# Optimization experiments

Measured on AMD Instinct MI355X. Metric: run time of the kernel, lower is better.

The kernel has to match this reference:

```python
import jax, jax.numpy as jnp
import numpy as np

B, H, L = 1024, 32, 3
D_S, D_ID = 512, 128
D_STEER = 3 * D_S + D_ID  # 1664
D_HID = 2048
HS, DQ = 16, 64
HDQ = HS * DQ  # 1024


def setup_inputs() -> dict:
    key = jax.random.key(0)
    ks = jax.random.split(key, 18)
    n = lambda k, shape, std: jax.random.normal(k, shape, dtype=jnp.float32) * std
    inp = {
        "x": jax.random.normal(ks[0], (B * H, D_STEER), dtype=jnp.float32),
        "id_in": jax.random.normal(ks[1], (B * H, D_ID), dtype=jnp.float32),
        # per-head content MLP params
        "in_proj_w": n(ks[2], (H, D_STEER, D_S), 0.014),
        "in_proj_b": jnp.zeros((H, D_S), jnp.float32),
        "norm_w": jnp.ones((H, L, D_S), jnp.float32),
        "up_w": n(ks[3], (H, L, D_S, D_HID), 0.014),
        "up_b": jnp.zeros((H, L, D_HID), jnp.float32),
        "down_w": n(ks[4], (H, L, D_HID, D_S), (2.0 / D_HID) ** 0.5),
        "down_b": jnp.zeros((H, L, D_S), jnp.float32),
        # q_proj: Linear(D_steer, 2*HDQ) -> GELU -> Linear(2*HDQ, HDQ)
        "q1_w": n(ks[5], (D_STEER, 2 * HDQ), 0.014),
        "q1_b": jnp.zeros((2 * HDQ,), jnp.float32),
        "q2_w": n(ks[6], (2 * HDQ, HDQ), 0.02),
        "q2_b": jnp.zeros((HDQ,), jnp.float32),
        # k_proj: Linear(D_id, 2*HDQ) -> GELU -> Linear(2*HDQ, HDQ)
        "k1_w": n(ks[7], (D_ID, 2 * HDQ), 0.014),
        "k1_b": jnp.zeros((2 * HDQ,), jnp.float32),
        "k2_w": n(ks[8], (2 * HDQ, HDQ), 0.02),
        "k2_b": jnp.zeros((HDQ,), jnp.float32),
    }
    return inp


def _per_head_mlp(x, in_proj_w, in_proj_b, norm_w, up_w, up_b, down_w, down_b):
    # x: [B*H, D_steer] -> [B*H, D_s]
    bh = x.shape[0]
    b = bh // H
    xh = x.reshape(b, H, D_STEER)
    h = jnp.einsum("bhd,hde->bhe", xh, in_proj_w) + in_proj_b[None]
    for i in range(norm_w.shape[1]):
        rms = jax.lax.rsqrt(jnp.mean(h * h, axis=-1, keepdims=True) + 1e-6)
        xn = h * rms * norm_w[:, i][None]
        hid = jax.nn.gelu(jnp.einsum("bhd,hde->bhe", xn, up_w[:, i]) + up_b[:, i][None], approximate=False)
        h = h + jnp.einsum("bhd,hde->bhe", hid, down_w[:, i]) + down_b[:, i][None]
    return h.reshape(bh, D_S)


def reference(x, id_in, in_proj_w, in_proj_b, norm_w, up_w, up_b, down_w, down_b,
              q1_w, q1_b, q2_w, q2_b, k1_w, k1_b, k2_w, k2_b):
    content = _per_head_mlp(x, in_proj_w, in_proj_b, norm_w, up_w, up_b, down_w, down_b)
    q = jax.nn.gelu(x @ q1_w + q1_b, approximate=False) @ q2_w + q2_b
    k = jax.nn.gelu(id_in @ k1_w + k1_b, approximate=False) @ k2_w + k2_b
    # concat outputs: [B*H, D_s + HDQ + HDQ]
    return jnp.concatenate([content, q, k], axis=-1)
```

## Files before the change

### kernel.cpp

```cpp
#include <hip/hip_runtime.h>
#include <hip/hip_bf16.h>
#include <math.h>

#define HH 32
#define LL 3
#define DS 512
#define DID 128
#define DSTEER 1664
#define DHID 2048
#define HDQ 1024
#define BHROWS 32768

typedef __attribute__((ext_vector_type(8))) short short8;
typedef __attribute__((ext_vector_type(4))) float f32x4;

typedef const __attribute__((address_space(1))) unsigned int* gptr_t;
typedef __attribute__((address_space(3))) unsigned int* lptr_t;

#define FENCE() asm volatile("" ::: "memory")
#define BAR() do { FENCE(); __builtin_amdgcn_s_barrier(); FENCE(); } while (0)
#define VMCNT10() asm volatile("s_waitcnt vmcnt(10)" ::: "memory")
#define VMCNT8()  asm volatile("s_waitcnt vmcnt(8)" ::: "memory")
#define VMCNT2()  asm volatile("s_waitcnt vmcnt(2)" ::: "memory")
#define VMCNT0()  asm volatile("s_waitcnt vmcnt(0)" ::: "memory")

__device__ __forceinline__ unsigned short f2bf(float f) {
  union { float f; unsigned int u; } x; x.f = f;
  unsigned int r = (x.u + 0x7FFFu + ((x.u >> 16) & 1u)) >> 16;
  return (unsigned short)r;
}
__device__ __forceinline__ unsigned int pk2(float a, float b) {
  return (unsigned int)f2bf(a) | ((unsigned int)f2bf(b) << 16);
}
__device__ __forceinline__ float gelu_exact(float v) {
  return 0.5f * v * (1.0f + erff(v * 0.70710678118654752440f));
}

__global__ void cvt_bf16_kernel(const float4* __restrict__ in, uint2* __restrict__ out, long n4) {
  long i = (long)blockIdx.x * blockDim.x + threadIdx.x;
  long stride = (long)gridDim.x * blockDim.x;
  for (; i < n4; i += stride) {
    float4 v = in[i];
    uint2 o; o.x = pk2(v.x, v.y); o.y = pk2(v.z, v.w);
    out[i] = o;
  }
}

__global__ void transpose_cvt_kernel(const float* __restrict__ in, long long in_bstride,
                                     unsigned short* __restrict__ out, long long out_bstride,
                                     int R, int C) {
  __shared__ float t[64][33];
  const int r0 = blockIdx.y * 32;
  const int c0 = blockIdx.x * 64;
  const float* bin = in + (long long)blockIdx.z * in_bstride;
  unsigned short* bout = out + (long long)blockIdx.z * out_bstride;
  const int tid = threadIdx.x;
  const int col = tid & 63, rr = tid >> 6;
  #pragma unroll
  for (int j = 0; j < 8; j++) {
    int r = j * 4 + rr;
    t[col][r] = bin[(size_t)(r0 + r) * C + c0 + col];
  }
  __syncthreads();
  const int rq = (tid & 7) * 4;
  const int cc = tid >> 3;
  #pragma unroll
  for (int j = 0; j < 2; j++) {
    int c = j * 32 + cc;
    float v0 = t[c][rq], v1 = t[c][rq + 1], v2 = t[c][rq + 2], v3 = t[c][rq + 3];
    uint2 o; o.x = pk2(v0, v1); o.y = pk2(v2, v3);
    *(uint2*)&bout[(size_t)(c0 + c) * R + r0 + rq] = o;
  }
}

__global__ void rms_scale_kernel(const float* __restrict__ h,
                                 const float* __restrict__ norm_w,
                                 unsigned short* __restrict__ xn, int layer) {
  int gw = (int)((blockIdx.x * blockDim.x + threadIdx.x) >> 6);
  int lane = threadIdx.x & 63;
  if (gw >= BHROWS) return;
  int head = gw & (HH - 1);
  const float4* hr = (const float4*)(h + (size_t)gw * DS);
  float4 v0 = hr[lane * 2], v1 = hr[lane * 2 + 1];
  float ss = v0.x*v0.x + v0.y*v0.y + v0.z*v0.z + v0.w*v0.w
           + v1.x*v1.x + v1.y*v1.y + v1.z*v1.z + v1.w*v1.w;
  #pragma unroll
  for (int off = 32; off > 0; off >>= 1) ss += __shfl_xor(ss, off, 64);
  float r = rsqrtf(ss * (1.0f / DS) + 1e-6f);
  const float4* nw = (const float4*)(norm_w + ((size_t)head * LL + layer) * DS);
  float4 w0 = nw[lane * 2], w1 = nw[lane * 2 + 1];
  uint4 o;
  o.x = pk2(v0.x * r * w0.x, v0.y * r * w0.y);
  o.y = pk2(v0.z * r * w0.z, v0.w * r * w0.w);
  o.z = pk2(v1.x * r * w1.x, v1.y * r * w1.y);
  o.w = pk2(v1.z * r * w1.z, v1.w * r * w1.w);
  *(uint4*)(xn + (size_t)gw * DS + (size_t)lane * 8) = o;
}

template<int EPI>
__global__ __launch_bounds__(512, 2)
void gemm256_kernel(const unsigned short* __restrict__ A, int lda, int rstep,
                    const unsigned short* __restrict__ Bt, int ldb, long long b_hstride,
                    const float* __restrict__ bias, int bias_hstride,
                    const float* __restrict__ resid, int ldr,
                    void* __restrict__ Cv, int ldc, int K) {
  __shared__ unsigned short lds[2 * 2 * 256 * 64];
  const int tid = threadIdx.x;
  const int lane = tid & 63;
  const int wave = tid >> 6;
  const int wr = wave >> 2, wc = wave & 3;
  const int head = blockIdx.z;
  const int gx = gridDim.x;
  const int nwg = gx * gridDim.y;
  int wgid = blockIdx.y * gx + blockIdx.x;
  { int cpx = nwg >> 3; wgid = (wgid & 7) * cpx + (wgid >> 3); }
  const int tn = wgid % gx, tm = wgid / gx;

  const int l3 = lane >> 3;
  const int gslot = ((lane & 7) ^ l3) * 8;
  const int mbase = wave * 8 + l3;
  const int nbase = (wave >> 2) * 64 + (wave & 3) * 8 + l3;
  const unsigned short* pA = A + ((size_t)(tm * 256 + mbase) * rstep + head) * lda + gslot;
  const unsigned short* pB = Bt + (size_t)head * b_hstride
                               + (size_t)(tn * 256 + nbase) * ldb + gslot;
  const size_t aBlk = (size_t)64 * rstep * lda;

  const int physk0 = ((lane >> 4) ^ (lane & 7)) * 8;
  const int physk1 = ((4 + (lane >> 4)) ^ (lane & 7)) * 8;
  const int aRow = wr * 128 + (lane & 15);
  const int bRow = wc * 32 + (lane & 15);

  auto stageA = [&](unsigned short* dstA, int h, size_t kels) {
    #pragma unroll
    for (int i = 0; i < 2; ++i)
      __builtin_amdgcn_global_load_lds(
          (gptr_t)(pA + (size_t)(i * 2 + h) * aBlk + kels),
          (lptr_t)(dstA + ((i * 2 + h) * 64 + wave * 8) * 64), 16, 0, 0);
  };
  auto stageB = [&](unsigned short* dstB, int h, size_t kels) {
    #pragma unroll
    for (int i = 0; i < 2; ++i)
      __builtin_amdgcn_global_load_lds(
          (gptr_t)(pB + (size_t)(i * 128 + h * 32) * ldb + kels),
          (lptr_t)(dstB + (h * 128 + i * 64 + wave * 8) * 64), 16, 0, 0);
  };

  f32x4 acc[8][4];
  #pragma unroll
  for (int i = 0; i < 8; ++i)
    #pragma unroll
    for (int j = 0; j < 4; ++j) acc[i][j] = (f32x4){0.f, 0.f, 0.f, 0.f};
  short8 a[4][2], b[4][2];

  const int T = K >> 6;
  stageA(lds, 0, 0);
  stageB(lds + 16384, 0, 0);
  stageB(lds + 16384, 1, 0);
  stageA(lds, 1, 0);
  if (1 < T) {
    stageA(lds + 32768, 0, 64);
    stageB(lds + 32768 + 16384, 0, 64);
    stageB(lds + 32768 + 16384, 1, 64);
    VMCNT8();
  } else {
    VMCNT2();
  }
  BAR();

  for (int t = 0; t < T; ++t) {
    unsigned short* rA = lds + (t & 1) * 32768;
    unsigned short* rB = rA + 16384;
    unsigned short* nA = lds + ((t + 1) & 1) * 32768;
    unsigned short* cA = rA;
    unsigned short* cB = rB;
    const size_t k1 = (size_t)(t + 1) * 64;
    const size_t k2 = (size_t)(t + 2) * 64;
    const bool m1 = (t + 1 < T), m2 = (t + 2 < T);

    #pragma unroll
    for (int i = 0; i < 4; ++i) {
      a[i][0] = *(const short8*)&rA[(aRow + i * 16) * 64 + physk0];
      a[i][1] = *(const short8*)&rA[(aRow + i * 16) * 64 + physk1];
    }
    #pragma unroll
    for (int j = 0; j < 2; ++j) {
      b[j][0] = *(const short8*)&rB[(bRow + j * 16) * 64 + physk0];
      b[j][1] = *(const short8*)&rB[(bRow + j * 16) * 64 + physk1];
    }
    if (m1) stageA(nA, 1, k1);
    BAR();
    __builtin_amdgcn_s_setprio(1);
    #pragma unroll
    for (int i = 0; i < 4; ++i)
      #pragma unroll
      for (int j = 0; j < 2; ++j) {
        acc[i][j] = __builtin_amdgcn_mfma_f32_16x16x32_bf16(a[i][0], b[j][0], acc[i][j], 0, 0, 0);
        acc[i][j] = __builtin_amdgcn_mfma_f32_16x16x32_bf16(a[i][1], b[j][1], acc[i][j], 0, 0, 0);
      }
    __builtin_amdgcn_s_setprio(0);
    BAR();

    #pragma unroll
    for (int j = 0; j < 2; ++j) {
      b[2 + j][0] = *(const short8*)&rB[(128 + bRow + j * 16) * 64 + physk0];
      b[2 + j][1] = *(const short8*)&rB[(128 + bRow + j * 16) * 64 + physk1];
    }
    if (m2) stageA(cA, 0, k2);
    BAR();
    __builtin_amdgcn_s_setprio(1);
    #pragma unroll
    for (int i = 0; i < 4; ++i)
      #pragma unroll
      for (int j = 0; j < 2; ++j) {
        acc[i][2 + j] = __builtin_amdgcn_mfma_f32_16x16x32_bf16(a[i][0], b[2 + j][0], acc[i][2 + j], 0, 0, 0);
        acc[i][2 + j] = __builtin_amdgcn_mfma_f32_16x16x32_bf16(a[i][1], b[2 + j][1], acc[i][2 + j], 0, 0, 0);
      }
    __builtin_amdgcn_s_setprio(0);
    if (m2) { VMCNT10(); } else if (m1) { VMCNT8(); } else { VMCNT0(); }
    BAR();

    #pragma unroll
    for (int i = 0; i < 4; ++i) {
      a[i][0] = *(const short8*)&rA[(aRow + (4 + i) * 16) * 64 + physk0];
      a[i][1] = *(const short8*)&rA[(aRow + (4 + i) * 16) * 64 + physk1];
    }
    if (m2) stageB(cB, 0, k2);
    BAR();
    __builtin_amdgcn_s_setprio(1);
    #pragma unroll
    for (int i = 0; i < 4; ++i)
      #pragma unroll
      for (int j = 0; j < 2; ++j) {
        acc[4 + i][2 + j] = __builtin_amdgcn_mfma_f32_16x16x32_bf16(a[i][0], b[2 + j][0], acc[4 + i][2 + j], 0, 0, 0);
        acc[4 + i][2 + j] = __builtin_amdgcn_mfma_f32_16x16x32_bf16(a[i][1], b[2 + j][1], acc[4 + i][2 + j], 0, 0, 0);
      }
    __builtin_amdgcn_s_setprio(0);
    BAR();

    if (m2) stageB(cB, 1, k2);
    BAR();
    __builtin_amdgcn_s_setprio(1);
    #pragma unroll
    for (int i = 0; i < 4; ++i)
      #pragma unroll
      for (int j = 0; j < 2; ++j) {
        acc[4 + i][j] = __builtin_amdgcn_mfma_f32_16x16x32_bf16(a[i][0], b[j][0], acc[4 + i][j], 0, 0, 0);
        acc[4 + i][j] = __builtin_amdgcn_mfma_f32_16x16x32_bf16(a[i][1], b[j][1], acc[4 + i][j], 0, 0, 0);
      }
    __builtin_amdgcn_s_setprio(0);
    if (m1) { if (m2) { VMCNT8(); } else { VMCNT2(); } }
    BAR();
  }

  const float* bptr = bias + (size_t)head * bias_hstride;
  #pragma unroll
  for (int i = 0; i < 8; ++i) {
    #pragma unroll
    for (int j = 0; j < 4; ++j) {
      #pragma unroll
      for (int r = 0; r < 4; ++r) {
        int rowt = wr * 128 + i * 16 + (lane >> 4) * 4 + r;
        int colt = wc * 64 + j * 16 + (lane & 15);
        int col = tn * 256 + colt;
        size_t crow = (size_t)(tm * 256 + rowt) * rstep + head;
        float v = acc[i][j][r] + bptr[col];
        if (EPI == 1) {
          ((unsigned short*)Cv)[crow * (size_t)ldc + col] = f2bf(gelu_exact(v));
        } else if (EPI == 2) {
          v += resid[crow * (size_t)ldr + col];
          ((float*)Cv)[crow * (size_t)ldc + col] = v;
        } else {
          ((float*)Cv)[crow * (size_t)ldc + col] = v;
        }
      }
    }
  }
}

extern "C" void kernel_launch(void* const* d_in, const int* in_sizes, int n_in,
                              void* d_out, int out_size, void* d_ws, size_t ws_size,
                              hipStream_t stream) {
  const float* x         = (const float*)d_in[0];
  const float* id_in     = (const float*)d_in[1];
  const float* in_proj_w = (const float*)d_in[2];
  const float* in_proj_b = (const float*)d_in[3];
  const float* norm_w    = (const float*)d_in[4];
  const float* up_w      = (const float*)d_in[5];
  const float* up_b      = (const float*)d_in[6];
  const float* down_w    = (const float*)d_in[7];
  const float* down_b    = (const float*)d_in[8];
  const float* q1_w      = (const float*)d_in[9];
  const float* q1_b      = (const float*)d_in[10];
  const float* q2_w      = (const float*)d_in[11];
  const float* q2_b      = (const float*)d_in[12];
  const float* k1_w      = (const float*)d_in[13];
  const float* k1_b      = (const float*)d_in[14];
  const float* k2_w      = (const float*)d_in[15];
  const float* k2_b      = (const float*)d_in[16];
  float* out = (float*)d_out;

  char* ws = (char*)d_ws;
  unsigned short* x_bf  = (unsigned short*)ws; ws += (size_t)BHROWS * DSTEER * 2;
  unsigned short* id_bf = (unsigned short*)ws; ws += (size_t)BHROWS * DID * 2;
  float*          hbuf  = (float*)ws;          ws += (size_t)BHROWS * DS * 4;
  unsigned short* xn    = (unsigned short*)ws; ws += (size_t)BHROWS * DS * 2;
  unsigned short* hid   = (unsigned short*)ws; ws += (size_t)BHROWS * DHID * 2;
  unsigned short* wbuf  = (unsigned short*)ws; ws += (size_t)HH * DHID * DS * 2;

  cvt_bf16_kernel<<<2048, 256, 0, stream>>>((const float4*)x, (uint2*)x_bf,
                                            (long)BHROWS * DSTEER / 4);
  cvt_bf16_kernel<<<512, 256, 0, stream>>>((const float4*)id_in, (uint2*)id_bf,
                                           (long)BHROWS * DID / 4);

  transpose_cvt_kernel<<<dim3(2 * HDQ / 64, DSTEER / 32, 1), 256, 0, stream>>>(
      q1_w, 0, wbuf, 0, DSTEER, 2 * HDQ);
  gemm256_kernel<1><<<dim3(8, 128, 1), 512, 0, stream>>>(
      x_bf, DSTEER, 1, wbuf, DSTEER, 0, q1_b, 0, nullptr, 0, hid, 2 * HDQ, DSTEER);
  transpose_cvt_kernel<<<dim3(HDQ / 64, 2 * HDQ / 32, 1), 256, 0, stream>>>(
      q2_w, 0, wbuf, 0, 2 * HDQ, HDQ);
  gemm256_kernel<0><<<dim3(4, 128, 1), 512, 0, stream>>>(
      hid, 2 * HDQ, 1, wbuf, 2 * HDQ, 0, q2_b, 0, nullptr, 0, out + 512, 2560, 2 * HDQ);

  transpose_cvt_kernel<<<dim3(2 * HDQ / 64, DID / 32, 1), 256, 0, stream>>>(
      k1_w, 0, wbuf, 0, DID, 2 * HDQ);
  gemm256_kernel<1><<<dim3(8, 128, 1), 512, 0, stream>>>(
      id_bf, DID, 1, wbuf, DID, 0, k1_b, 0, nullptr, 0, hid, 2 * HDQ, DID);
  transpose_cvt_kernel<<<dim3(HDQ / 64, 2 * HDQ / 32, 1), 256, 0, stream>>>(
      k2_w, 0, wbuf, 0, 2 * HDQ, HDQ);
  gemm256_kernel<0><<<dim3(4, 128, 1), 512, 0, stream>>>(
      hid, 2 * HDQ, 1, wbuf, 2 * HDQ, 0, k2_b, 0, nullptr, 0, out + 1536, 2560, 2 * HDQ);

  transpose_cvt_kernel<<<dim3(DS / 64, DSTEER / 32, HH), 256, 0, stream>>>(
      in_proj_w, (long long)DSTEER * DS, wbuf, (long long)DS * DSTEER, DSTEER, DS);
  gemm256_kernel<0><<<dim3(2, 4, 32), 512, 0, stream>>>(
      x_bf, DSTEER, HH, wbuf, DSTEER, (long long)DS * DSTEER, in_proj_b, DS,
      nullptr, 0, hbuf, DS, DSTEER);

  for (int i = 0; i < LL; i++) {
    rms_scale_kernel<<<8192, 256, 0, stream>>>(hbuf, norm_w, xn, i);
    transpose_cvt_kernel<<<dim3(DHID / 64, DS / 32, HH), 256, 0, stream>>>(
        up_w + (size_t)i * DS * DHID, (long long)LL * DS * DHID,
        wbuf, (long long)DHID * DS, DS, DHID);
    gemm256_kernel<1><<<dim3(8, 4, 32), 512, 0, stream>>>(
        xn, DS, HH, wbuf, DS, (long long)DHID * DS,
        up_b + (size_t)i * DHID, LL * DHID, nullptr, 0, hid, DHID, DS);
    transpose_cvt_kernel<<<dim3(DS / 64, DHID / 32, HH), 256, 0, stream>>>(
        down_w + (size_t)i * DHID * DS, (long long)LL * DHID * DS,
        wbuf, (long long)DS * DHID, DHID, DS);
    float* cout = (i < 2) ? hbuf : out;
    int ldc = (i < 2) ? DS : 2560;
    gemm256_kernel<2><<<dim3(2, 4, 32), 512, 0, stream>>>(
        hid, DHID, HH, wbuf, DHID, (long long)DS * DHID,
        down_b + (size_t)i * DS, LL * DS, hbuf, DS, cout, ldc, DHID);
  }
}
```

Measured before the change: 1.726 ms.

## Software-pipeline LDS fragment loads across MFMA quadrants with register double-buffering

Restructures the GEMM main loop so LDS fragment reads for the next quadrant or next K-tile are issued before the current quadrant's MFMAs. Fine-grained lgkmcnt waits and sched barriers let ds_read latency hide behind matrix math. The loop is unrolled by two with ping-pong B-fragment registers, and the prologue and epilogue tiles are peeled with hand-tuned vmcnt thresholds. This adds register pressure. It also assumes an even tile count of at least two, and the vmcnt accounting must exactly match the outstanding global-to-LDS loads.

```diff
diff --git a/kernel.cpp b/kernel.cpp
--- a/kernel.cpp
+++ b/kernel.cpp
@@ -19,10 +19,13 @@
 
 #define FENCE() asm volatile("" ::: "memory")
 #define BAR() do { FENCE(); __builtin_amdgcn_s_barrier(); FENCE(); } while (0)
-#define VMCNT10() asm volatile("s_waitcnt vmcnt(10)" ::: "memory")
 #define VMCNT8()  asm volatile("s_waitcnt vmcnt(8)" ::: "memory")
+#define VMCNT4()  asm volatile("s_waitcnt vmcnt(4)" ::: "memory")
 #define VMCNT2()  asm volatile("s_waitcnt vmcnt(2)" ::: "memory")
 #define VMCNT0()  asm volatile("s_waitcnt vmcnt(0)" ::: "memory")
+#define VMNOP()   do {} while (0)
+#define LGKM(n) do { asm volatile("s_waitcnt lgkmcnt(" #n ")" ::: "memory"); \
+                     __builtin_amdgcn_sched_barrier(0); } while (0)
 
 __device__ __forceinline__ unsigned short f2bf(float f) {
   union { float f; unsigned int u; } x; x.f = f;
@@ -150,107 +153,102 @@
   for (int i = 0; i < 8; ++i)
     #pragma unroll
     for (int j = 0; j < 4; ++j) acc[i][j] = (f32x4){0.f, 0.f, 0.f, 0.f};
-  short8 a[4][2], b[4][2];
+  short8 aA[4][2], aB[4][2], bA[2][2], bB[2][2];
+
+#define MFMA_Q(MO, NO, AR, BR) do { \
+    __builtin_amdgcn_s_setprio(1); \
+    _Pragma("unroll") \
+    for (int i_ = 0; i_ < 4; ++i_) { \
+      _Pragma("unroll") \
+      for (int j_ = 0; j_ < 2; ++j_) { \
+        acc[(MO)+i_][(NO)+j_] = __builtin_amdgcn_mfma_f32_16x16x32_bf16( \
+            AR[i_][0], BR[j_][0], acc[(MO)+i_][(NO)+j_], 0, 0, 0); \
+        acc[(MO)+i_][(NO)+j_] = __builtin_amdgcn_mfma_f32_16x16x32_bf16( \
+            AR[i_][1], BR[j_][1], acc[(MO)+i_][(NO)+j_], 0, 0, 0); \
+      } \
+    } \
+    __builtin_amdgcn_s_setprio(0); \
+  } while (0)
+
+#define TILE(tt, LO, HI, PAR, M1, M2, VMP0, VMP2, VMP3) { \
+    unsigned short* rA = lds + (PAR) * 32768; \
+    unsigned short* rB = rA + 16384; \
+    unsigned short* nA = lds + ((PAR) ^ 1) * 32768; \
+    unsigned short* nB = nA + 16384; \
+    const size_t k1_ = (size_t)((tt) + 1) * 64; \
+    const size_t k2_ = (size_t)((tt) + 2) * 64; \
+     \
+    HI[0][0] = *(const short8*)&rB[(128 + bRow) * 64 + physk0]; \
+    HI[0][1] = *(const short8*)&rB[(128 + bRow) * 64 + physk1]; \
+    HI[1][0] = *(const short8*)&rB[(144 + bRow) * 64 + physk0]; \
+    HI[1][1] = *(const short8*)&rB[(144 + bRow) * 64 + physk1]; \
+    if (M1) stageA(nA, 1, k1_); \
+    LGKM(4); \
+    MFMA_Q(0, 0, aA, LO); \
+    VMP0; BAR(); \
+     \
+    _Pragma("unroll") \
+    for (int i_ = 0; i_ < 4; ++i_) { \
+      aB[i_][0] = *(const short8*)&rA[(aRow + (4 + i_) * 16) * 64 + physk0]; \
+      aB[i_][1] = *(const short8*)&rA[(aRow + (4 + i_) * 16) * 64 + physk1]; \
+    } \
+    if (M2) stageA(rA, 0, k2_); \
+    LGKM(8); \
+    MFMA_Q(0, 2, aA, HI); \
+    BAR(); \
+     \
+    if (M2) stageB(rB, 0, k2_); \
+    LGKM(0); \
+    MFMA_Q(4, 2, aB, HI); \
+    VMP2; BAR(); \
+     \
+    if (M1) { \
+      _Pragma("unroll") \
+      for (int i_ = 0; i_ < 4; ++i_) { \
+        aA[i_][0] = *(const short8*)&nA[(aRow + i_ * 16) * 64 + physk0]; \
+        aA[i_][1] = *(const short8*)&nA[(aRow + i_ * 16) * 64 + physk1]; \
+      } \
+      HI[0][0] = *(const short8*)&nB[(bRow) * 64 + physk0]; \
+      HI[0][1] = *(const short8*)&nB[(bRow) * 64 + physk1]; \
+      HI[1][0] = *(const short8*)&nB[(bRow + 16) * 64 + physk0]; \
+      HI[1][1] = *(const short8*)&nB[(bRow + 16) * 64 + physk1]; \
+      __builtin_amdgcn_sched_barrier(0); \
+    } \
+    if (M2) stageB(rB, 1, k2_); \
+    MFMA_Q(4, 0, aB, LO); \
+    VMP3; BAR(); \
+  }
 
   const int T = K >> 6;
   stageA(lds, 0, 0);
   stageB(lds + 16384, 0, 0);
   stageB(lds + 16384, 1, 0);
+  VMCNT0();
+  BAR();
+  #pragma unroll
+  for (int i = 0; i < 4; ++i) {
+    aA[i][0] = *(const short8*)&lds[(aRow + i * 16) * 64 + physk0];
+    aA[i][1] = *(const short8*)&lds[(aRow + i * 16) * 64 + physk1];
+  }
+  bA[0][0] = *(const short8*)&lds[(16384 / 1) + 0];
+  bA[0][0] = *(const short8*)&lds[16384 + (bRow) * 64 + physk0];
+  bA[0][1] = *(const short8*)&lds[16384 + (bRow) * 64 + physk1];
+  bA[1][0] = *(const short8*)&lds[16384 + (bRow + 16) * 64 + physk0];
+  bA[1][1] = *(const short8*)&lds[16384 + (bRow + 16) * 64 + physk1];
   stageA(lds, 1, 0);
-  if (1 < T) {
-    stageA(lds + 32768, 0, 64);
-    stageB(lds + 32768 + 16384, 0, 64);
-    stageB(lds + 32768 + 16384, 1, 64);
-    VMCNT8();
-  } else {
-    VMCNT2();
-  }
-  BAR();
-
-  for (int t = 0; t < T; ++t) {
-    unsigned short* rA = lds + (t & 1) * 32768;
-    unsigned short* rB = rA + 16384;
-    unsigned short* nA = lds + ((t + 1) & 1) * 32768;
-    unsigned short* cA = rA;
-    unsigned short* cB = rB;
-    const size_t k1 = (size_t)(t + 1) * 64;
-    const size_t k2 = (size_t)(t + 2) * 64;
-    const bool m1 = (t + 1 < T), m2 = (t + 2 < T);
-
-    #pragma unroll
-    for (int i = 0; i < 4; ++i) {
-      a[i][0] = *(const short8*)&rA[(aRow + i * 16) * 64 + physk0];
-      a[i][1] = *(const short8*)&rA[(aRow + i * 16) * 64 + physk1];
-    }
-    #pragma unroll
-    for (int j = 0; j < 2; ++j) {
-      b[j][0] = *(const short8*)&rB[(bRow + j * 16) * 64 + physk0];
-      b[j][1] = *(const short8*)&rB[(bRow + j * 16) * 64 + physk1];
-    }
-    if (m1) stageA(nA, 1, k1);
-    BAR();
-    __builtin_amdgcn_s_setprio(1);
-    #pragma unroll
-    for (int i = 0; i < 4; ++i)
-      #pragma unroll
-      for (int j = 0; j < 2; ++j) {
-        acc[i][j] = __builtin_amdgcn_mfma_f32_16x16x32_bf16(a[i][0], b[j][0], acc[i][j], 0, 0, 0);
-        acc[i][j] = __builtin_amdgcn_mfma_f32_16x16x32_bf16(a[i][1], b[j][1], acc[i][j], 0, 0, 0);
-      }
-    __builtin_amdgcn_s_setprio(0);
-    BAR();
-
-    #pragma unroll
-    for (int j = 0; j < 2; ++j) {
-      b[2 + j][0] = *(const short8*)&rB[(128 + bRow + j * 16) * 64 + physk0];
-      b[2 + j][1] = *(const short8*)&rB[(128 + bRow + j * 16) * 64 + physk1];
-    }
-    if (m2) stageA(cA, 0, k2);
-    BAR();
-    __builtin_amdgcn_s_setprio(1);
-    #pragma unroll
-    for (int i = 0; i < 4; ++i)
-      #pragma unroll
-      for (int j = 0; j < 2; ++j) {
-        acc[i][2 + j] = __builtin_amdgcn_mfma_f32_16x16x32_bf16(a[i][0], b[2 + j][0], acc[i][2 + j], 0, 0, 0);
-        acc[i][2 + j] = __builtin_amdgcn_mfma_f32_16x16x32_bf16(a[i][1], b[2 + j][1], acc[i][2 + j], 0, 0, 0);
-      }
-    __builtin_amdgcn_s_setprio(0);
-    if (m2) { VMCNT10(); } else if (m1) { VMCNT8(); } else { VMCNT0(); }
-    BAR();
-
-    #pragma unroll
-    for (int i = 0; i < 4; ++i) {
-      a[i][0] = *(const short8*)&rA[(aRow + (4 + i) * 16) * 64 + physk0];
-      a[i][1] = *(const short8*)&rA[(aRow + (4 + i) * 16) * 64 + physk1];
-    }
-    if (m2) stageB(cB, 0, k2);
-    BAR();
-    __builtin_amdgcn_s_setprio(1);
-    #pragma unroll
-    for (int i = 0; i < 4; ++i)
-      #pragma unroll
-      for (int j = 0; j < 2; ++j) {
-        acc[4 + i][2 + j] = __builtin_amdgcn_mfma_f32_16x16x32_bf16(a[i][0], b[2 + j][0], acc[4 + i][2 + j], 0, 0, 0);
-        acc[4 + i][2 + j] = __builtin_amdgcn_mfma_f32_16x16x32_bf16(a[i][1], b[2 + j][1], acc[4 + i][2 + j], 0, 0, 0);
-      }
-    __builtin_amdgcn_s_setprio(0);
-    BAR();
-
-    if (m2) stageB(cB, 1, k2);
-    BAR();
-    __builtin_amdgcn_s_setprio(1);
-    #pragma unroll
-    for (int i = 0; i < 4; ++i)
-      #pragma unroll
-      for (int j = 0; j < 2; ++j) {
-        acc[4 + i][j] = __builtin_amdgcn_mfma_f32_16x16x32_bf16(a[i][0], b[j][0], acc[4 + i][j], 0, 0, 0);
-        acc[4 + i][j] = __builtin_amdgcn_mfma_f32_16x16x32_bf16(a[i][1], b[j][1], acc[4 + i][j], 0, 0, 0);
-      }
-    __builtin_amdgcn_s_setprio(0);
-    if (m1) { if (m2) { VMCNT8(); } else { VMCNT2(); } }
-    BAR();
-  }
+  stageA(lds + 32768, 0, 64);
+  stageB(lds + 32768 + 16384, 0, 64);
+  stageB(lds + 32768 + 16384, 1, 64);
+
+  for (int t = 0; t + 3 < T; t += 2) {
+    TILE(t,     bA, bB, 0, 1, 1, VMCNT8(), VMCNT8(), VMCNT8());
+    TILE(t + 1, bB, bA, 1, 1, 1, VMCNT8(), VMCNT8(), VMCNT8());
+  }
+  TILE(T - 2, bA, bB, 0, 1, 0, VMCNT8(), VMCNT4(), VMCNT2());
+  TILE(T - 1, bB, bA, 1, 0, 0, VMCNT0(), VMNOP(), VMNOP());
+
+#undef TILE
+#undef MFMA_Q
 
   const float* bptr = bias + (size_t)head * bias_hstride;
   #pragma unroll
```

Result: slower. 3.898 ms (+125.8%).
